# Kernel optimization log

Hardware: AMD Instinct MI355X
Metric: run time of the kernel (lower is better)

## Reference

```python
import jax, jax.numpy as jnp
import numpy as np

B, S, D, H = 4, 2048, 1024, 16
HD = D // H


def setup_inputs() -> dict:
    key = jax.random.key(0)
    ks = jax.random.split(key, 5)
    scale = 0.02
    return {
        "x": jax.random.normal(ks[0], (B, S, D), dtype=jnp.float32),
        "Wq": jax.random.normal(ks[1], (D, D), dtype=jnp.float32) * scale,
        "Wk": jax.random.normal(ks[2], (D, D), dtype=jnp.float32) * scale,
        "Wv": jax.random.normal(ks[3], (D, D), dtype=jnp.float32) * scale,
        "Wo": jax.random.normal(ks[4], (D, D), dtype=jnp.float32) * scale,
    }


def reference(x, Wq, Wk, Wv, Wo):
    b, s, d = x.shape
    # Linear layers (torch Linear: y = x @ W.T), no bias
    q = jnp.einsum('bsd,ed->bse', x, Wq).reshape(b, s, H, HD).transpose(0, 2, 1, 3)
    k = jnp.einsum('bsd,ed->bse', x, Wk).reshape(b, s, H, HD).transpose(0, 2, 1, 3)
    v = jnp.einsum('bsd,ed->bse', x, Wv).reshape(b, s, H, HD).transpose(0, 2, 1, 3)
    # [B,H,S,S] attention scores
    scores = jnp.einsum('bhqd,bhkd->bhqk', q, k)
    causal = jnp.tril(jnp.ones((s, s), dtype=bool))
    scores = jnp.where(causal, scores, -jnp.inf)
    # faithful to source: mask first, then scale, then softmax
    weights = jax.nn.softmax(scores / jnp.sqrt(jnp.float32(HD)), axis=-1)
    # dropout p=0.0 (eval): identity
    ctx = jnp.einsum('bhqk,bhkd->bhqd', weights, v)
    ctx = ctx.transpose(0, 2, 1, 3).reshape(b, s, d)
    return jnp.einsum('bsd,ed->bse', ctx, Wo)
```

## Files before the change

kernel.cpp:

```cpp
#include <hip/hip_runtime.h>
#include <math.h>

typedef unsigned short u16;
typedef __attribute__((ext_vector_type(8))) short short8;
typedef __attribute__((ext_vector_type(4))) float f32x4;
typedef __attribute__((ext_vector_type(16))) float f32x16;
typedef __attribute__((ext_vector_type(4))) unsigned int u32x4;

constexpr int Bb = 4, S_LEN = 2048, DMODEL = 1024, NH = 16;
constexpr int MTOT = Bb * S_LEN;

#define QSCALE 0.18033688011112042f

__device__ __forceinline__ u16 f2bf(float f) {
    union { float f; unsigned u; } v; v.f = f;
    unsigned r = v.u + 0x7FFFu + ((v.u >> 16) & 1u);
    return (u16)(r >> 16);
}

__device__ __forceinline__ float exp2_fast(float x) {
#if __has_builtin(__builtin_amdgcn_exp2f)
    return __builtin_amdgcn_exp2f(x);
#else
    float r; asm("v_exp_f32 %0, %1" : "=v"(r) : "v"(x)); return r;
#endif
}

__device__ __forceinline__ unsigned pk_bf16(float s0, float s1) {
    unsigned pk;
    asm("v_cvt_pk_bf16_f32 %0, %1, %2" : "=v"(pk) : "v"(s0), "v"(s1));
    return pk;
}

__device__ __forceinline__ void load_lds16(const void* g, void* l) {
    __builtin_amdgcn_global_load_lds(
        (const __attribute__((address_space(1))) unsigned int*)g,
        (__attribute__((address_space(3))) unsigned int*)l, 16, 0, 0);
}

__global__ __launch_bounds__(256)
void cvt_all(const float* __restrict__ x,
             const float* __restrict__ w0, const float* __restrict__ w1,
             const float* __restrict__ w2, const float* __restrict__ w3,
             u16* __restrict__ xb, u16* __restrict__ b0, u16* __restrict__ b1,
             u16* __restrict__ b2, u16* __restrict__ b3)
{
    int gid = blockIdx.x * 256 + threadIdx.x;
    constexpr int NXo = (MTOT * DMODEL) / 8;
    constexpr int NWo = (DMODEL * DMODEL) / 8;
    const float* s; u16* d; int o;
    float sc = 1.0f;
    if (gid < NXo) { s = x; d = xb; o = gid; }
    else {
        int t = gid - NXo;
        int w = t >> 17;
        o = t & (NWo - 1);
        s = (w == 0) ? w0 : (w == 1) ? w1 : (w == 2) ? w2 : w3;
        d = (w == 0) ? b0 : (w == 1) ? b1 : (w == 2) ? b2 : b3;
        if (w == 0) sc = QSCALE;
    }
    const float4* sp = (const float4*)(s + (size_t)o * 8);
    float4 a = sp[0], bq = sp[1];
    short8 ov;
    ov[0] = (short)f2bf(a.x * sc);  ov[1] = (short)f2bf(a.y * sc);
    ov[2] = (short)f2bf(a.z * sc);  ov[3] = (short)f2bf(a.w * sc);
    ov[4] = (short)f2bf(bq.x * sc); ov[5] = (short)f2bf(bq.y * sc);
    ov[6] = (short)f2bf(bq.z * sc); ov[7] = (short)f2bf(bq.w * sc);
    *(short8*)(d + (size_t)o * 8) = ov;
}

__global__ __launch_bounds__(256, 2)
void gemm_bt(const u16* __restrict__ X,
             const u16* __restrict__ W0, const u16* __restrict__ W1, const u16* __restrict__ W2,
             u16* __restrict__ Y0, u16* __restrict__ Y1, u16* __restrict__ Y2,
             int M, int N, int K)
{
    const u16* W = (blockIdx.z == 0) ? W0 : (blockIdx.z == 1) ? W1 : W2;
    u16*       Y = (blockIdx.z == 0) ? Y0 : (blockIdx.z == 1) ? Y1 : Y2;

    __shared__ __align__(16) u16 lA[128 * 64];
    __shared__ __align__(16) u16 lB[128 * 64];

    const int tid  = threadIdx.x;
    const int wave = tid >> 6;
    const int lane = tid & 63;
    const int qd   = lane >> 4;
    const int c    = lane & 15;
    const int tm   = blockIdx.x * 128;
    const int tn   = blockIdx.y * 128;
    const int wm   = (wave >> 1) * 64;
    const int wn   = (wave & 1) * 64;

    f32x4 acc[4][4] = {};

    for (int k0 = 0; k0 < K; k0 += 64) {
        if (k0) __syncthreads();
#pragma unroll
        for (int it = 0; it < 4; ++it) {
            int chunk = it * 256 + tid;
            int row = chunk >> 3, hc = chunk & 7;
            load_lds16(X + (size_t)(tm + row) * K + k0 + hc * 8,
                       (char*)lA + (it * 256 + wave * 64) * 16);
            load_lds16(W + (size_t)(tn + row) * K + k0 + hc * 8,
                       (char*)lB + (it * 256 + wave * 64) * 16);
        }
        __syncthreads();

#pragma unroll
        for (int kk = 0; kk < 64; kk += 32) {
            short8 a[4], b[4];
#pragma unroll
            for (int i = 0; i < 4; ++i) {
                a[i] = *(const short8*)&lA[(wm + i * 16 + c) * 64 + kk + qd * 8];
                b[i] = *(const short8*)&lB[(wn + i * 16 + c) * 64 + kk + qd * 8];
            }
#pragma unroll
            for (int mi = 0; mi < 4; ++mi)
#pragma unroll
                for (int ni = 0; ni < 4; ++ni)
                    acc[mi][ni] = __builtin_amdgcn_mfma_f32_16x16x32_bf16(
                        a[mi], b[ni], acc[mi][ni], 0, 0, 0);
        }
    }

#pragma unroll
    for (int mi = 0; mi < 4; ++mi)
#pragma unroll
        for (int ni = 0; ni < 4; ++ni)
#pragma unroll
            for (int r = 0; r < 4; r += 2) {
                unsigned pk = pk_bf16(acc[mi][ni][r], acc[mi][ni][r + 1]);
                int row = tm + wm + mi * 16 + qd * 4 + r;
                int col = tn + wn + ni * 16 + c;
                Y[(size_t)row * N + col]       = (u16)(pk & 0xffffu);
                Y[(size_t)(row + 1) * N + col] = (u16)(pk >> 16);
            }
}

__global__ __launch_bounds__(256, 2)
void gemm_bt_f32(const u16* __restrict__ X, const u16* __restrict__ W,
                 float* __restrict__ Y, int M, int N, int K)
{
    __shared__ __align__(16) u16 lA[128 * 64];
    __shared__ __align__(16) u16 lB[128 * 64];

    const int tid  = threadIdx.x;
    const int wave = tid >> 6;
    const int lane = tid & 63;
    const int qd   = lane >> 4;
    const int c    = lane & 15;
    const int tm   = blockIdx.x * 128;
    const int tn   = blockIdx.y * 128;
    const int wm   = (wave >> 1) * 64;
    const int wn   = (wave & 1) * 64;

    f32x4 acc[4][4] = {};

    for (int k0 = 0; k0 < K; k0 += 64) {
        if (k0) __syncthreads();
#pragma unroll
        for (int it = 0; it < 4; ++it) {
            int chunk = it * 256 + tid;
            int row = chunk >> 3, hc = chunk & 7;
            load_lds16(X + (size_t)(tm + row) * K + k0 + hc * 8,
                       (char*)lA + (it * 256 + wave * 64) * 16);
            load_lds16(W + (size_t)(tn + row) * K + k0 + hc * 8,
                       (char*)lB + (it * 256 + wave * 64) * 16);
        }
        __syncthreads();

#pragma unroll
        for (int kk = 0; kk < 64; kk += 32) {
            short8 a[4], b[4];
#pragma unroll
            for (int i = 0; i < 4; ++i) {
                a[i] = *(const short8*)&lA[(wm + i * 16 + c) * 64 + kk + qd * 8];
                b[i] = *(const short8*)&lB[(wn + i * 16 + c) * 64 + kk + qd * 8];
            }
#pragma unroll
            for (int mi = 0; mi < 4; ++mi)
#pragma unroll
                for (int ni = 0; ni < 4; ++ni)
                    acc[mi][ni] = __builtin_amdgcn_mfma_f32_16x16x32_bf16(
                        a[mi], b[ni], acc[mi][ni], 0, 0, 0);
        }
    }

#pragma unroll
    for (int mi = 0; mi < 4; ++mi)
#pragma unroll
        for (int ni = 0; ni < 4; ++ni)
#pragma unroll
            for (int r = 0; r < 4; ++r) {
                int row = tm + wm + mi * 16 + qd * 4 + r;
                int col = tn + wn + ni * 16 + c;
                Y[(size_t)row * N + col] = acc[mi][ni][r];
            }
}

__global__ __launch_bounds__(256)
void transpose_v(const u16* __restrict__ V, u16* __restrict__ VT)
{
    const int sblk = blockIdx.x;
    const int bh   = blockIdx.y;
    const int b = bh >> 4, h = bh & 15;
    __shared__ __align__(16) u16 lT[64][72];

    const int t = threadIdx.x;
#pragma unroll
    for (int it = 0; it < 2; ++it) {
        int chunk = it * 256 + t;
        int si = chunk >> 3, hc = chunk & 7;
        short8 val = *(const short8*)&V[(size_t)(b * S_LEN + sblk * 64 + si) * DMODEL + h * 64 + hc * 8];
        *(short8*)&lT[si][hc * 8] = val;
    }
    __syncthreads();
#pragma unroll
    for (int it = 0; it < 2; ++it) {
        int chunk = it * 256 + t;
        int hd = chunk >> 3, sc = chunk & 7;
        short8 o;
#pragma unroll
        for (int j = 0; j < 8; ++j) o[j] = (short)lT[sc * 8 + j][hd];
        *(short8*)&VT[(size_t)(bh * 64 + hd) * S_LEN + sblk * 64 + sc * 8] = o;
    }
}

__global__ __launch_bounds__(512, 2)
void attention(const u16* __restrict__ Q, const u16* __restrict__ K,
               const u16* __restrict__ VT, u16* __restrict__ CTX)
{
    const int i  = blockIdx.x;
    const int j  = i & 255;
    const int bh = j >> 2;
    const int t  = j & 3;
    const int qt = (i >> 8) ? t : (7 - t);
    const int b = bh >> 4, h = bh & 15;

    __shared__ __align__(16) u16 lK[2][64 * 64];
    __shared__ __align__(16) u16 lV[2][64 * 64];

    const int tid = threadIdx.x, wave = tid >> 6, lane = tid & 63;
    const int l31 = lane & 31, hi = lane >> 5;
    const int wrow = wave * 32;
    const int srow = tid >> 3, shc = tid & 7;
    const int shcs = shc ^ (srow & 7);
    const int rxk  = l31 & 7;
    const size_t kbase = (size_t)(b * S_LEN) * DMODEL + h * 64;
    const size_t vbase = (size_t)(bh * 64) * S_LEN;

    const int q0 = qt * 256;
    const int nkv = 4 * qt + 4;
    const int qrg = q0 + wrow + l31;

    short8 qf[4];
#pragma unroll
    for (int ks = 0; ks < 4; ++ks)
        qf[ks] = *(const short8*)&Q[(size_t)(b * S_LEN + qrg) * DMODEL
                                    + h * 64 + ks * 16 + hi * 8];

    f32x16 oacc0 = {}, oacc1 = {};
    float psum = 0.f;

    load_lds16(K + kbase + (size_t)srow * DMODEL + shcs * 8,
               (char*)lK[0] + wave * 1024);
    load_lds16(VT + vbase + (size_t)srow * S_LEN + shcs * 8,
               (char*)lV[0] + wave * 1024);

    for (int kt = 0; kt < nkv; ++kt) {
        const int cur = kt & 1;
        const int k0 = kt * 64;

        __builtin_amdgcn_s_barrier();
        if (kt + 1 < nkv) {
            const int kn = (kt + 1) * 64;
            load_lds16(K + kbase + (size_t)(kn + srow) * DMODEL + shcs * 8,
                       (char*)lK[cur ^ 1] + wave * 1024);
            load_lds16(VT + vbase + (size_t)srow * S_LEN + kn + shcs * 8,
                       (char*)lV[cur ^ 1] + wave * 1024);
            asm volatile("s_waitcnt vmcnt(2)" ::: "memory");
        } else {
            asm volatile("s_waitcnt vmcnt(0)" ::: "memory");
        }
        __builtin_amdgcn_sched_barrier(0);
        __builtin_amdgcn_s_barrier();
        __builtin_amdgcn_sched_barrier(0);

        if (k0 <= q0 + wrow + 31) {
            f32x16 s0 = {}, s1 = {};
            __builtin_amdgcn_s_setprio(1);
#pragma unroll
            for (int hs = 0; hs < 4; ++hs) {
                const int sl = ((hs * 2 + hi) ^ rxk) << 3;
                short8 kf0 = *(const short8*)&lK[cur][l31 * 64 + sl];
                short8 kf1 = *(const short8*)&lK[cur][(32 + l31) * 64 + sl];
                s0 = __builtin_amdgcn_mfma_f32_32x32x16_bf16(kf0, qf[hs], s0, 0, 0, 0);
                s1 = __builtin_amdgcn_mfma_f32_32x32x16_bf16(kf1, qf[hs], s1, 0, 0, 0);
            }
            __builtin_amdgcn_s_setprio(0);

            float pva[16], pvb[16];
            if (k0 + 63 > q0 + wrow) {
                const int lim = qrg - k0 - 4 * hi;
#pragma unroll
                for (int r = 0; r < 16; ++r) {
                    const int ka = (r & 3) + 8 * (r >> 2);
                    pva[r] = (ka > lim)      ? -1.0e38f : s0[r];
                    pvb[r] = (ka + 32 > lim) ? -1.0e38f : s1[r];
                }
            } else {
#pragma unroll
                for (int r = 0; r < 16; ++r) { pva[r] = s0[r]; pvb[r] = s1[r]; }
            }
#pragma unroll
            for (int r = 0; r < 16; ++r) {
                pva[r] = exp2_fast(fminf(pva[r], 86.0f));
                pvb[r] = exp2_fast(fminf(pvb[r], 86.0f));
                psum += pva[r] + pvb[r];
            }
            unsigned own0[8], own1[8];
#pragma unroll
            for (int q = 0; q < 8; ++q) {
                own0[q] = pk_bf16(pva[2 * q], pva[2 * q + 1]);
                own1[q] = pk_bf16(pvb[2 * q], pvb[2 * q + 1]);
            }

            short8 paf[4];
#pragma unroll
            for (int f = 0; f < 4; ++f) {
                const unsigned* own = (f < 2) ? own0 : own1;
                const int base = (f & 1) * 4;
                unsigned a0 = own[base + 0], b0 = own[base + 2];
                unsigned a1 = own[base + 1], b1 = own[base + 3];
                asm("v_permlane32_swap_b32 %0, %1" : "+v"(a0), "+v"(b0));
                asm("v_permlane32_swap_b32 %0, %1" : "+v"(a1), "+v"(b1));
                u32x4 w; w[0] = a0; w[1] = a1; w[2] = b0; w[3] = b1;
                paf[f] = __builtin_bit_cast(short8, w);
            }

            __builtin_amdgcn_s_setprio(1);
#pragma unroll
            for (int ks = 0; ks < 4; ++ks) {
                const int vsl = ((ks * 2 + hi) ^ rxk) << 3;
                short8 vf0 = *(const short8*)&lV[cur][l31 * 64 + vsl];
                short8 vf1 = *(const short8*)&lV[cur][(32 + l31) * 64 + vsl];
                oacc0 = __builtin_amdgcn_mfma_f32_32x32x16_bf16(paf[ks], vf0, oacc0, 0, 0, 0);
                oacc1 = __builtin_amdgcn_mfma_f32_32x32x16_bf16(paf[ks], vf1, oacc1, 0, 0, 0);
            }
            __builtin_amdgcn_s_setprio(0);
        }
    }

    float pt = psum + __shfl_xor(psum, 32);
#pragma unroll
    for (int r = 0; r < 16; ++r) {
        const int orow = (r & 3) + 8 * (r >> 2) + 4 * hi;
        float inv = 1.0f / __shfl(pt, orow);
        const int rowg = q0 + wrow + orow;
        size_t base = (size_t)(b * S_LEN + rowg) * DMODEL + h * 64;
        unsigned pk = pk_bf16(oacc0[r] * inv, oacc1[r] * inv);
        CTX[base + l31]      = (u16)(pk & 0xffffu);
        CTX[base + 32 + l31] = (u16)(pk >> 16);
    }
}

extern "C" void kernel_launch(void* const* d_in, const int* in_sizes, int n_in,
                              void* d_out, int out_size, void* d_ws, size_t ws_size,
                              hipStream_t stream)
{
    const size_t MB = 1024 * 1024;
    char* ws = (char*)d_ws;
    if (ws_size < 72 * MB + 64) return;

    u16* xb  = (u16*)ws;
    u16* wb0 = (u16*)(ws + 16 * MB);
    u16* wb1 = (u16*)(ws + 18 * MB);
    u16* wb2 = (u16*)(ws + 20 * MB);
    u16* wb3 = (u16*)(ws + 22 * MB);
    u16* q   = (u16*)(ws + 24 * MB);
    u16* k   = (u16*)(ws + 40 * MB);
    u16* v   = (u16*)(ws + 56 * MB);
    u16* vt  = xb;
    u16* ctx = v;
    float* out = (float*)d_out;

    constexpr int NCVT = (MTOT * DMODEL + 4 * DMODEL * DMODEL) / 8 / 256;

    cvt_all<<<NCVT, 256, 0, stream>>>(
        (const float*)d_in[0], (const float*)d_in[1], (const float*)d_in[2],
        (const float*)d_in[3], (const float*)d_in[4], xb, wb0, wb1, wb2, wb3);

    gemm_bt<<<dim3(MTOT / 128, DMODEL / 128, 3), 256, 0, stream>>>(
        xb, wb0, wb1, wb2, q, k, v, MTOT, DMODEL, DMODEL);
    transpose_v<<<dim3(S_LEN / 64, Bb * NH), 256, 0, stream>>>(v, vt);
    attention<<<512, 512, 0, stream>>>(q, k, vt, ctx);
    gemm_bt_f32<<<dim3(MTOT / 128, DMODEL / 128, 1), 256, 0, stream>>>(
        ctx, wb3, out, MTOT, DMODEL, DMODEL);
}
```

Before: 248.8 us.

## Fuse V transpose into QKV GEMM epilogue via swizzled LDS staging

The V projection blocks now write their output tile transposed directly into the VT layout. Each wave stages its 64x64 accumulator tile in LDS with an XOR swizzle and reads it back column-wise, which removes the separate transpose_v kernel and its extra global read/write pass over V. Workspace aliasing is rearranged so ctx reuses the xb buffer. The cost is a slightly heavier epilogue for a third of the GEMM blocks and some LDS bank traffic on the strided reads.

```diff
diff --git a/kernel.cpp b/kernel.cpp
--- a/kernel.cpp
+++ b/kernel.cpp
@@ -72,14 +72,15 @@
 __global__ __launch_bounds__(256, 2)
 void gemm_bt(const u16* __restrict__ X,
              const u16* __restrict__ W0, const u16* __restrict__ W1, const u16* __restrict__ W2,
-             u16* __restrict__ Y0, u16* __restrict__ Y1, u16* __restrict__ Y2,
+             u16* __restrict__ Y0, u16* __restrict__ Y1,
+             u16* __restrict__ VT,
              int M, int N, int K)
 {
     const u16* W = (blockIdx.z == 0) ? W0 : (blockIdx.z == 1) ? W1 : W2;
-    u16*       Y = (blockIdx.z == 0) ? Y0 : (blockIdx.z == 1) ? Y1 : Y2;
-
-    __shared__ __align__(16) u16 lA[128 * 64];
-    __shared__ __align__(16) u16 lB[128 * 64];
+
+    __shared__ __align__(16) u16 lds[2 * 128 * 64];
+    u16* lA = lds;
+    u16* lB = lds + 128 * 64;
 
     const int tid  = threadIdx.x;
     const int wave = tid >> 6;
@@ -123,18 +124,53 @@
         }
     }
 
-#pragma unroll
-    for (int mi = 0; mi < 4; ++mi)
-#pragma unroll
-        for (int ni = 0; ni < 4; ++ni)
-#pragma unroll
-            for (int r = 0; r < 4; r += 2) {
-                unsigned pk = pk_bf16(acc[mi][ni][r], acc[mi][ni][r + 1]);
-                int row = tm + wm + mi * 16 + qd * 4 + r;
-                int col = tn + wn + ni * 16 + c;
-                Y[(size_t)row * N + col]       = (u16)(pk & 0xffffu);
-                Y[(size_t)(row + 1) * N + col] = (u16)(pk >> 16);
-            }
+    if (blockIdx.z != 2) {
+        u16* Y = (blockIdx.z == 0) ? Y0 : Y1;
+#pragma unroll
+        for (int mi = 0; mi < 4; ++mi)
+#pragma unroll
+            for (int ni = 0; ni < 4; ++ni)
+#pragma unroll
+                for (int r = 0; r < 4; r += 2) {
+                    unsigned pk = pk_bf16(acc[mi][ni][r], acc[mi][ni][r + 1]);
+                    int row = tm + wm + mi * 16 + qd * 4 + r;
+                    int col = tn + wn + ni * 16 + c;
+                    Y[(size_t)row * N + col]       = (u16)(pk & 0xffffu);
+                    Y[(size_t)(row + 1) * N + col] = (u16)(pk >> 16);
+                }
+    } else {
+        __syncthreads();
+        u16* Tw = lds + wave * 4096;
+#pragma unroll
+        for (int mi = 0; mi < 4; ++mi)
+#pragma unroll
+            for (int ni = 0; ni < 4; ++ni)
+#pragma unroll
+                for (int r = 0; r < 4; r += 2) {
+                    unsigned pk = pk_bf16(acc[mi][ni][r], acc[mi][ni][r + 1]);
+                    int r0 = mi * 16 + qd * 4 + r;
+                    int cl = ni * 16 + c;
+                    Tw[r0 * 64       + (cl ^ ((r0 << 1) & 0x38))]        = (u16)(pk & 0xffffu);
+                    Tw[(r0 + 1) * 64 + (cl ^ (((r0 + 1) << 1) & 0x38))]  = (u16)(pk >> 16);
+                }
+        asm volatile("s_waitcnt lgkmcnt(0)" ::: "memory");
+
+        const int b2   = tm >> 11;
+        const int smb  = (tm & 2047) + wm;
+        const int hgl  = (tn + wn) >> 6;
+        const int sc8  = lane & 7;
+#pragma unroll
+        for (int it = 0; it < 8; ++it) {
+            int hd = it * 8 + (lane >> 3);
+            short8 o;
+#pragma unroll
+            for (int jj = 0; jj < 8; ++jj) {
+                int rr = sc8 * 8 + jj;
+                o[jj] = (short)Tw[rr * 64 + (hd ^ ((rr << 1) & 0x38))];
+            }
+            *(short8*)&VT[(size_t)((b2 * 16 + hgl) * 64 + hd) * S_LEN + smb + sc8 * 8] = o;
+        }
+    }
 }
 
 __global__ __launch_bounds__(256, 2)
@@ -196,34 +232,6 @@
                 int col = tn + wn + ni * 16 + c;
                 Y[(size_t)row * N + col] = acc[mi][ni][r];
             }
-}
-
-__global__ __launch_bounds__(256)
-void transpose_v(const u16* __restrict__ V, u16* __restrict__ VT)
-{
-    const int sblk = blockIdx.x;
-    const int bh   = blockIdx.y;
-    const int b = bh >> 4, h = bh & 15;
-    __shared__ __align__(16) u16 lT[64][72];
-
-    const int t = threadIdx.x;
-#pragma unroll
-    for (int it = 0; it < 2; ++it) {
-        int chunk = it * 256 + t;
-        int si = chunk >> 3, hc = chunk & 7;
-        short8 val = *(const short8*)&V[(size_t)(b * S_LEN + sblk * 64 + si) * DMODEL + h * 64 + hc * 8];
-        *(short8*)&lT[si][hc * 8] = val;
-    }
-    __syncthreads();
-#pragma unroll
-    for (int it = 0; it < 2; ++it) {
-        int chunk = it * 256 + t;
-        int hd = chunk >> 3, sc = chunk & 7;
-        short8 o;
-#pragma unroll
-        for (int j = 0; j < 8; ++j) o[j] = (short)lT[sc * 8 + j][hd];
-        *(short8*)&VT[(size_t)(bh * 64 + hd) * S_LEN + sblk * 64 + sc * 8] = o;
-    }
 }
 
 __global__ __launch_bounds__(512, 2)
@@ -379,9 +387,8 @@
     u16* wb3 = (u16*)(ws + 22 * MB);
     u16* q   = (u16*)(ws + 24 * MB);
     u16* k   = (u16*)(ws + 40 * MB);
-    u16* v   = (u16*)(ws + 56 * MB);
-    u16* vt  = xb;
-    u16* ctx = v;
+    u16* vt  = (u16*)(ws + 56 * MB);
+    u16* ctx = xb;
     float* out = (float*)d_out;
 
     constexpr int NCVT = (MTOT * DMODEL + 4 * DMODEL * DMODEL) / 8 / 256;
@@ -391,8 +398,7 @@
         (const float*)d_in[3], (const float*)d_in[4], xb, wb0, wb1, wb2, wb3);
 
     gemm_bt<<<dim3(MTOT / 128, DMODEL / 128, 3), 256, 0, stream>>>(
-        xb, wb0, wb1, wb2, q, k, v, MTOT, DMODEL, DMODEL);
-    transpose_v<<<dim3(S_LEN / 64, Bb * NH), 256, 0, stream>>>(v, vt);
+        xb, wb0, wb1, wb2, q, k, vt, MTOT, DMODEL, DMODEL);
     attention<<<512, 512, 0, stream>>>(q, k, vt, ctx);
     gemm_bt_f32<<<dim3(MTOT / 128, DMODEL / 128, 1), 256, 0, stream>>>(
         ctx, wb3, out, MTOT, DMODEL, DMODEL);
```

Measured after the change: 245.2 us. Within noise of the previous version (-1.4%).
